# Kernel tuning notes

Measured on AMD Instinct MI355X. Metric: run time of the kernel, lower is better.

Reference implementation:

```python
import jax, jax.numpy as jnp
import numpy as np

T, B, IN, H, L = 512, 64, 1024, 1024, 2


def setup_inputs() -> dict:
    key = jax.random.key(0)
    ks = jax.random.split(key, 7)
    s = 1.0 / np.sqrt(H)
    return {
        "x": jax.random.normal(ks[0], (T, B, IN), jnp.float32),
        "h0": jax.random.normal(ks[1], (L, B, H), jnp.float32) * 0.1,
        "c0": jax.random.normal(ks[2], (L, B, H), jnp.float32) * 0.1,
        "W0": jax.random.uniform(ks[3], (4 * H, IN + H), jnp.float32, -s, s),
        "b0": jax.random.uniform(ks[4], (4 * H,), jnp.float32, -s, s),
        "W1": jax.random.uniform(ks[5], (4 * H, H + H), jnp.float32, -s, s),
        "b1": jax.random.uniform(ks[6], (4 * H,), jnp.float32, -s, s),
    }


def _cell(xin, h, c, W, b):
    # xin: [B, D], h/c: [B, H], W: [4H, D+H], b: [4H]
    xh = jnp.concatenate([xin, h], axis=1)
    gates = xh @ W.T + b
    i, f, g, o = jnp.split(gates, 4, axis=1)  # ingate, forgetgate, cellgate, outgate
    i = jax.nn.sigmoid(i)
    f = jax.nn.sigmoid(f)
    g = jnp.tanh(g)
    o = jax.nn.sigmoid(o)
    cy = i * g + f * c
    hy = o * jnp.tanh(cy)
    return hy, cy


def reference(x, h0, c0, W0, b0, W1, b1):
    Ws = [(W0, b0), (W1, b1)]

    def step(carry, xt):
        h, c = carry  # each [L, B, H]
        xin = xt
        hs, cs = [], []
        for k in range(L):
            W, b = Ws[k]
            hy, cy = _cell(xin, h[k], c[k], W, b)
            hs.append(hy)
            cs.append(cy)
            xin = hy
        return (jnp.stack(hs), jnp.stack(cs)), xin  # xin is last-layer h

    (h, c), hlast = jax.lax.scan(step, (h0, c0), x)
    return hlast, h, c
```

## Files before the change

### kernel.cpp

```cpp
#include <hip/hip_runtime.h>
#include <hip/hip_bf16.h>
#include <stdint.h>

#define TT 512
#define BB 64
#define HH 1024
#define BH 65536
#define KD 2048

typedef __attribute__((ext_vector_type(8))) short short8;
typedef __attribute__((ext_vector_type(4))) float f32x4;

__device__ __forceinline__ unsigned short f2bf(float f) {
  union { float f; unsigned int u; } v; v.f = f;
  unsigned int r = v.u + 0x7fffu + ((v.u >> 16) & 1u);
  return (unsigned short)(r >> 16);
}
__device__ __forceinline__ float bf2f(unsigned short u) {
  union { unsigned int u; float f; } v; v.u = ((unsigned int)u) << 16; return v.f;
}
__device__ __forceinline__ float fsig(float x)  { return 1.0f / (1.0f + __expf(-x)); }
__device__ __forceinline__ float ftanhf(float x){ return 1.0f - 2.0f / (__expf(2.0f * x) + 1.0f); }

__global__ void cvt_x_kernel(const float* __restrict__ x, unsigned short* __restrict__ xbf) {
  const int n4 = (TT * BB * 1024) / 4;
  int stride = gridDim.x * blockDim.x;
  for (int i = blockIdx.x * blockDim.x + threadIdx.x; i < n4; i += stride) {
    float4 v = ((const float4*)x)[i];
    unsigned long long p = (unsigned long long)f2bf(v.x)
        | ((unsigned long long)f2bf(v.y) << 16)
        | ((unsigned long long)f2bf(v.z) << 32)
        | ((unsigned long long)f2bf(v.w) << 48);
    ((unsigned long long*)xbf)[i] = p;
  }
}

__global__ void cvt_w_kernel(const float* __restrict__ W, unsigned short* __restrict__ Ws) {
  int idx = blockIdx.x * blockDim.x + threadIdx.x;
  int hi = idx & 3;
  int nr = (idx >> 2) & 31;
  int kk = (idx >> 7) & 63;
  int g  = idx >> 13;
  int q  = nr & 3;
  int jl = (nr >> 2) & 3;
  int nt = nr >> 4;
  int grow = (q << 10) + (g << 3) + (nt << 2) + jl;
  int k = ((kk < 32) ? (kk << 5) : (1024 + ((kk - 32) << 5))) + (hi << 3);
  const float* src = W + (size_t)grow * KD + k;
  float4 v0 = ((const float4*)src)[0];
  float4 v1 = ((const float4*)src)[1];
  unsigned long long p0 = (unsigned long long)f2bf(v0.x)
      | ((unsigned long long)f2bf(v0.y) << 16)
      | ((unsigned long long)f2bf(v0.z) << 32)
      | ((unsigned long long)f2bf(v0.w) << 48);
  unsigned long long p1 = (unsigned long long)f2bf(v1.x)
      | ((unsigned long long)f2bf(v1.y) << 16)
      | ((unsigned long long)f2bf(v1.z) << 32)
      | ((unsigned long long)f2bf(v1.w) << 48);
  unsigned long long* dst = (unsigned long long*)(Ws + ((size_t)g << 16) + (kk << 10) + (nr << 5) + (hi << 3));
  dst[0] = p0;
  dst[1] = p1;
}

__global__ void init_state_kernel(const float* __restrict__ h0in,
                                  unsigned short* h0s0, unsigned short* h1s0) {
  int i = blockIdx.x * blockDim.x + threadIdx.x;
  int m = i >> 10, c = i & 1023;
  int dst = ((c >> 3) << 9) + (m << 3) + (c & 7);
  h0s0[dst] = f2bf(h0in[i]);
  h1s0[dst] = f2bf(h0in[BH + i]);
}

__global__ void finalize_kernel(const unsigned short* __restrict__ h0hist,
                                const unsigned short* __restrict__ h1hist,
                                float* __restrict__ out) {
  const size_t NCH = (size_t)(TT + 2) * (BH / 8);
  size_t stride = (size_t)gridDim.x * blockDim.x;
  for (size_t i = (size_t)blockIdx.x * blockDim.x + threadIdx.x; i < NCH; i += stride) {
    int p  = (int)(i >> 13);
    int ci = (int)(i & 8191);
    int cb = ci >> 6, m = ci & 63;
    const unsigned short* src;
    size_t dbase;
    if (p < TT)       { src = h1hist + (size_t)(p + 1) * BH; dbase = (size_t)p * BH; }
    else if (p == TT) { src = h0hist + (size_t)TT * BH;      dbase = (size_t)TT * BH; }
    else              { src = h1hist + (size_t)TT * BH;      dbase = (size_t)TT * BH + BH; }
    const unsigned short* sp = src + ((size_t)ci << 3);
    ushort4 v0 = ((const ushort4*)sp)[0];
    ushort4 v1 = ((const ushort4*)sp)[1];
    float* dp = out + dbase + (m << 10) + (cb << 3);
    *(float4*)(dp)     = make_float4(bf2f(v0.x), bf2f(v0.y), bf2f(v0.z), bf2f(v0.w));
    *(float4*)(dp + 4) = make_float4(bf2f(v1.x), bf2f(v1.y), bf2f(v1.z), bf2f(v1.w));
  }
}

#define GLD(p)    __hip_atomic_load((p),  __ATOMIC_RELAXED, __HIP_MEMORY_SCOPE_AGENT)
#define GST(p, v) __hip_atomic_store((p), (v), __ATOMIC_RELAXED, __HIP_MEMORY_SCOPE_AGENT)

__device__ __forceinline__ void poll128(int* base) {
  for (;;) {
    int s = 0;
#pragma unroll
    for (int j = 0; j < 8; j++)
      s += GLD(base + (j << 6));
    if (s >= 128) return;
    __builtin_amdgcn_s_sleep(1);
  }
}

__global__ __launch_bounds__(512, 2) void lstm_persist(
    const unsigned short* __restrict__ W0s, const unsigned short* __restrict__ W1s,
    const float* __restrict__ b0, const float* __restrict__ b1,
    const unsigned short* __restrict__ xbf,
    unsigned short* h0hist, unsigned short* h1hist,
    const float* __restrict__ c0in, float* out, int* cnt)
{
  __shared__ short8 wlds[8192];
  __shared__ f32x4 pbuf[2][4][2][64];
  const int tid = threadIdx.x;
  const int bid = blockIdx.x;
  const int layer = bid >> 7;
  const int g = bid & 127;

  const unsigned short* Ws = layer ? W1s : W0s;
  const float* bias = layer ? b1 : b0;
  int* const cnt0 = cnt;
  int* const cnt1 = cnt + (TT << 9);

  {
    const short8* wsrc = (const short8*)(Ws + ((size_t)g << 16));
#pragma unroll
    for (int it = 0; it < 16; it++)
      wlds[tid + (it << 9)] = wsrc[tid + (it << 9)];
  }

  const int lane = tid & 63;
  const int w  = tid >> 6;
  const bool isA = (w < 4);
  const int mt = w & 3;
  const int m0 = mt << 4;
  const int n  = lane & 15;
  const int hi = lane >> 4;
  const short8* bbase0 = wlds + ((n << 2) + hi);
  const short8* bbase1 = wlds + (((16 + n) << 2) + hi);
  const int m = m0 + n;
  const int rowoff = (m << 10) + (hi << 3);
  const int bro = ((hi << 6) + m) << 3;
  const int col0 = (g << 3) + hi;
  const int col1 = col0 + 4;

  unsigned short* const myhist = (layer == 0) ? h0hist : h1hist;
  int* const mycnt = (layer == 0) ? cnt0 : cnt1;

  float bq[2][4];
  float creg[2];
  if (!isA) {
#pragma unroll
    for (int nt2 = 0; nt2 < 2; nt2++) {
      int col = nt2 ? col1 : col0;
#pragma unroll
      for (int qg = 0; qg < 4; qg++)
        bq[nt2][qg] = bias[(qg << 10) + col];
      creg[nt2] = c0in[(size_t)layer * BH + (m << 10) + col];
    }
  }
  __syncthreads();

  if (isA) {
    if (layer == 1) {
      if (lane == 0) poll128(cnt0);
      asm volatile("" ::: "memory");
    }
    f32x4 a0 = {0.f, 0.f, 0.f, 0.f}, a1 = {0.f, 0.f, 0.f, 0.f};
    if (layer == 0) {
      const unsigned short* asrc = xbf + rowoff;
      short8 ha[8];
#pragma unroll
      for (int j = 0; j < 8; j++) ha[j] = *(const short8*)(asrc + (j << 5));
#pragma unroll
      for (int blk = 0; blk < 4; blk++)
#pragma unroll
        for (int j = 0; j < 8; j++) {
          int kk = (blk << 3) + j;
          a0 = __builtin_amdgcn_mfma_f32_16x16x32_bf16(bbase0[kk << 7], ha[j], a0, 0, 0, 0);
          a1 = __builtin_amdgcn_mfma_f32_16x16x32_bf16(bbase1[kk << 7], ha[j], a1, 0, 0, 0);
          if (blk < 3) ha[j] = *(const short8*)(asrc + ((kk + 8) << 5));
        }
    } else {
      const unsigned short* asrc = h0hist + (size_t)BH + bro;
      short8 ha[8];
#pragma unroll
      for (int j = 0; j < 8; j++) ha[j] = *(const short8*)(asrc + (j << 11));
#pragma unroll
      for (int blk = 0; blk < 4; blk++)
#pragma unroll
        for (int j = 0; j < 8; j++) {
          int kk = (blk << 3) + j;
          a0 = __builtin_amdgcn_mfma_f32_16x16x32_bf16(bbase0[kk << 7], ha[j], a0, 0, 0, 0);
          a1 = __builtin_amdgcn_mfma_f32_16x16x32_bf16(bbase1[kk << 7], ha[j], a1, 0, 0, 0);
          if (blk < 3) ha[j] = *(const short8*)(asrc + ((kk + 8) << 11));
        }
    }
    pbuf[0][mt][0][lane] = a0;
    pbuf[0][mt][1][lane] = a1;
  }
  __syncthreads();

  for (int s = 0; s < TT; s++) {
    if (isA) {
      if (s + 1 < TT) {
        f32x4 a0 = {0.f, 0.f, 0.f, 0.f}, a1 = {0.f, 0.f, 0.f, 0.f};
        if (layer == 0) {
          const unsigned short* asrc = xbf + (size_t)(s + 1) * BH + rowoff;
          short8 ha[8];
#pragma unroll
          for (int j = 0; j < 8; j++) ha[j] = *(const short8*)(asrc + (j << 5));
#pragma unroll
          for (int blk = 0; blk < 4; blk++)
#pragma unroll
            for (int j = 0; j < 8; j++) {
              int kk = (blk << 3) + j;
              a0 = __builtin_amdgcn_mfma_f32_16x16x32_bf16(bbase0[kk << 7], ha[j], a0, 0, 0, 0);
              a1 = __builtin_amdgcn_mfma_f32_16x16x32_bf16(bbase1[kk << 7], ha[j], a1, 0, 0, 0);
              if (blk < 3) ha[j] = *(const short8*)(asrc + ((kk + 8) << 5));
            }
        } else {
          if (lane == 0) poll128(cnt0 + ((s + 1) << 9));
          asm volatile("" ::: "memory");
          const unsigned short* asrc = h0hist + (size_t)(s + 2) * BH + bro;
          short8 ha[8];
#pragma unroll
          for (int j = 0; j < 8; j++) ha[j] = *(const short8*)(asrc + (j << 11));
#pragma unroll
          for (int blk = 0; blk < 4; blk++)
#pragma unroll
            for (int j = 0; j < 8; j++) {
              int kk = (blk << 3) + j;
              a0 = __builtin_amdgcn_mfma_f32_16x16x32_bf16(bbase0[kk << 7], ha[j], a0, 0, 0, 0);
              a1 = __builtin_amdgcn_mfma_f32_16x16x32_bf16(bbase1[kk << 7], ha[j], a1, 0, 0, 0);
              if (blk < 3) ha[j] = *(const short8*)(asrc + ((kk + 8) << 11));
            }
        }
        int buf = (s + 1) & 1;
        pbuf[buf][mt][0][lane] = a0;
        pbuf[buf][mt][1][lane] = a1;
      }
    } else {
      if (s >= 1) {
        if (lane == 0) poll128(mycnt + ((s - 1) << 9));
        asm volatile("" ::: "memory");
      }
      f32x4 acc0 = pbuf[s & 1][mt][0][lane];
      f32x4 acc1 = pbuf[s & 1][mt][1][lane];
      const unsigned short* inB = myhist + (size_t)s * BH + bro;
      short8 ha[8];
#pragma unroll
      for (int j = 0; j < 8; j++) ha[j] = *(const short8*)(inB + (j << 11));
#pragma unroll
      for (int blk = 0; blk < 4; blk++)
#pragma unroll
        for (int j = 0; j < 8; j++) {
          int kk = (blk << 3) + j;
          acc0 = __builtin_amdgcn_mfma_f32_16x16x32_bf16(bbase0[(32 + kk) << 7], ha[j], acc0, 0, 0, 0);
          acc1 = __builtin_amdgcn_mfma_f32_16x16x32_bf16(bbase1[(32 + kk) << 7], ha[j], acc1, 0, 0, 0);
          if (blk < 3) ha[j] = *(const short8*)(inB + ((kk + 8) << 11));
        }

      unsigned short* hbb = myhist + (size_t)(s + 1) * BH + (((g << 6) + m) << 3);
#pragma unroll
      for (int nt2 = 0; nt2 < 2; nt2++) {
        f32x4 acc = nt2 ? acc1 : acc0;
        float ig = fsig(acc[0] + bq[nt2][0]);
        float fg = fsig(acc[1] + bq[nt2][1]);
        float gg = ftanhf(acc[2] + bq[nt2][2]);
        float og = fsig(acc[3] + bq[nt2][3]);
        float cn = ig * gg + fg * creg[nt2];
        float hn = og * ftanhf(cn);
        creg[nt2] = cn;
        GST(hbb + (nt2 << 2) + hi, f2bf(hn));
      }
    }

    __syncthreads();
    if (tid == 0) atomicAdd(mycnt + (s << 9) + ((g & 7) << 6), 1);

    if (!isA && s == TT - 1) {
#pragma unroll
      for (int nt2 = 0; nt2 < 2; nt2++) {
        const int col = nt2 ? col1 : col0;
        out[(size_t)TT * BH + (size_t)(2 + layer) * BH + (m << 10) + col] = creg[nt2];
      }
    }
  }
}

extern "C" void kernel_launch(void* const* d_in, const int* in_sizes, int n_in,
                              void* d_out, int out_size, void* d_ws, size_t ws_size,
                              hipStream_t stream) {
  (void)in_sizes; (void)n_in; (void)out_size; (void)ws_size;
  const float* x    = (const float*)d_in[0];
  const float* h0in = (const float*)d_in[1];
  const float* c0in = (const float*)d_in[2];
  const float* W0   = (const float*)d_in[3];
  const float* b0   = (const float*)d_in[4];
  const float* W1   = (const float*)d_in[5];
  const float* b1   = (const float*)d_in[6];
  float* out = (float*)d_out;

  char* ws = (char*)d_ws;
  const size_t HIST = (size_t)(TT + 1) * BH * sizeof(unsigned short);
  unsigned short* Xbf    = (unsigned short*)(ws);
  unsigned short* W0s    = (unsigned short*)(ws + 67108864);
  unsigned short* W1s    = (unsigned short*)(ws + 83886080);
  unsigned short* h0hist = (unsigned short*)(ws + 100663296);
  unsigned short* h1hist = (unsigned short*)(ws + 100663296 + HIST);
  int* cnt               = (int*)(ws + 100663296 + 2 * HIST);

  const size_t CNT_BYTES = (size_t)2 * TT * 512 * sizeof(int);
  hipMemsetAsync(cnt, 0, CNT_BYTES, stream);
  cvt_x_kernel<<<2048, 256, 0, stream>>>(x, Xbf);
  cvt_w_kernel<<<4096, 256, 0, stream>>>(W0, W0s);
  cvt_w_kernel<<<4096, 256, 0, stream>>>(W1, W1s);
  init_state_kernel<<<256, 256, 0, stream>>>(h0in, h0hist, h1hist);

  lstm_persist<<<256, 512, 0, stream>>>(W0s, W1s, b0, b1, Xbf,
                                        h0hist, h1hist, c0in, out, cnt);

  finalize_kernel<<<2048, 256, 0, stream>>>(h0hist, h1hist, out);
}
```

Before: 4.203 ms.

## Prefetch next-step A-wave inputs into registers and use a custom barrier

```diff
diff --git a/kernel.cpp b/kernel.cpp
--- a/kernel.cpp
+++ b/kernel.cpp
@@ -166,6 +166,7 @@
   }
   __syncthreads();
 
+  short8 xa[16], xb[16];
   if (isA) {
     if (layer == 1) {
       if (lane == 0) poll128(cnt0);
@@ -203,6 +204,21 @@
     }
     pbuf[0][mt][0][lane] = a0;
     pbuf[0][mt][1][lane] = a1;
+    if (layer == 0) {
+      const unsigned short* asrc = xbf + (size_t)BH + rowoff;
+#pragma unroll
+      for (int j = 0; j < 16; j++) xa[j] = *(const short8*)(asrc + (j << 5));
+#pragma unroll
+      for (int j = 0; j < 16; j++) xb[j] = *(const short8*)(asrc + ((16 + j) << 5));
+    } else {
+      if (lane == 0) poll128(cnt0 + (1 << 9));
+      asm volatile("" ::: "memory");
+      const unsigned short* asrc = h0hist + (size_t)2 * BH + bro;
+#pragma unroll
+      for (int j = 0; j < 16; j++) xa[j] = *(const short8*)(asrc + (j << 11));
+#pragma unroll
+      for (int j = 0; j < 16; j++) xb[j] = *(const short8*)(asrc + ((16 + j) << 11));
+    }
   }
   __syncthreads();
 
@@ -210,40 +226,36 @@
     if (isA) {
       if (s + 1 < TT) {
         f32x4 a0 = {0.f, 0.f, 0.f, 0.f}, a1 = {0.f, 0.f, 0.f, 0.f};
-        if (layer == 0) {
-          const unsigned short* asrc = xbf + (size_t)(s + 1) * BH + rowoff;
-          short8 ha[8];
-#pragma unroll
-          for (int j = 0; j < 8; j++) ha[j] = *(const short8*)(asrc + (j << 5));
-#pragma unroll
-          for (int blk = 0; blk < 4; blk++)
-#pragma unroll
-            for (int j = 0; j < 8; j++) {
-              int kk = (blk << 3) + j;
-              a0 = __builtin_amdgcn_mfma_f32_16x16x32_bf16(bbase0[kk << 7], ha[j], a0, 0, 0, 0);
-              a1 = __builtin_amdgcn_mfma_f32_16x16x32_bf16(bbase1[kk << 7], ha[j], a1, 0, 0, 0);
-              if (blk < 3) ha[j] = *(const short8*)(asrc + ((kk + 8) << 5));
-            }
-        } else {
-          if (lane == 0) poll128(cnt0 + ((s + 1) << 9));
-          asm volatile("" ::: "memory");
-          const unsigned short* asrc = h0hist + (size_t)(s + 2) * BH + bro;
-          short8 ha[8];
-#pragma unroll
-          for (int j = 0; j < 8; j++) ha[j] = *(const short8*)(asrc + (j << 11));
-#pragma unroll
-          for (int blk = 0; blk < 4; blk++)
-#pragma unroll
-            for (int j = 0; j < 8; j++) {
-              int kk = (blk << 3) + j;
-              a0 = __builtin_amdgcn_mfma_f32_16x16x32_bf16(bbase0[kk << 7], ha[j], a0, 0, 0, 0);
-              a1 = __builtin_amdgcn_mfma_f32_16x16x32_bf16(bbase1[kk << 7], ha[j], a1, 0, 0, 0);
-              if (blk < 3) ha[j] = *(const short8*)(asrc + ((kk + 8) << 11));
-            }
+#pragma unroll
+        for (int j = 0; j < 16; j++) {
+          a0 = __builtin_amdgcn_mfma_f32_16x16x32_bf16(bbase0[j << 7], xa[j], a0, 0, 0, 0);
+          a1 = __builtin_amdgcn_mfma_f32_16x16x32_bf16(bbase1[j << 7], xa[j], a1, 0, 0, 0);
+        }
+#pragma unroll
+        for (int j = 0; j < 16; j++) {
+          a0 = __builtin_amdgcn_mfma_f32_16x16x32_bf16(bbase0[(16 + j) << 7], xb[j], a0, 0, 0, 0);
+          a1 = __builtin_amdgcn_mfma_f32_16x16x32_bf16(bbase1[(16 + j) << 7], xb[j], a1, 0, 0, 0);
         }
         int buf = (s + 1) & 1;
         pbuf[buf][mt][0][lane] = a0;
         pbuf[buf][mt][1][lane] = a1;
+      }
+      if (s + 2 < TT) {
+        if (layer == 0) {
+          const unsigned short* asrc = xbf + (size_t)(s + 2) * BH + rowoff;
+#pragma unroll
+          for (int j = 0; j < 16; j++) xa[j] = *(const short8*)(asrc + (j << 5));
+#pragma unroll
+          for (int j = 0; j < 16; j++) xb[j] = *(const short8*)(asrc + ((16 + j) << 5));
+        } else {
+          if (lane == 0) poll128(cnt0 + ((s + 2) << 9));
+          asm volatile("" ::: "memory");
+          const unsigned short* asrc = h0hist + (size_t)(s + 3) * BH + bro;
+#pragma unroll
+          for (int j = 0; j < 16; j++) xa[j] = *(const short8*)(asrc + (j << 11));
+#pragma unroll
+          for (int j = 0; j < 16; j++) xb[j] = *(const short8*)(asrc + ((16 + j) << 11));
+        }
       }
     } else {
       if (s >= 1) {
@@ -279,10 +291,14 @@
         creg[nt2] = cn;
         GST(hbb + (nt2 << 2) + hi, f2bf(hn));
       }
-    }
-
-    __syncthreads();
-    if (tid == 0) atomicAdd(mycnt + (s << 9) + ((g & 7) << 6), 1);
+      asm volatile("s_waitcnt vmcnt(0)" ::: "memory");
+    }
+
+    asm volatile("s_waitcnt lgkmcnt(0)" ::: "memory");
+    __builtin_amdgcn_sched_barrier(0);
+    __builtin_amdgcn_s_barrier();
+    __builtin_amdgcn_sched_barrier(0);
+    if (tid == 256) atomicAdd(mycnt + (s << 9) + ((g & 7) << 6), 1);
 
     if (!isA && s == TT - 1) {
 #pragma unroll
```

After: 5.266 ms. 1.25x slower.

## Replace recurrent counter barrier with per-wave byte-tag flags and deepen load prefetch

Applied to the files above, without the earlier changes.

```diff
diff --git a/kernel.cpp b/kernel.cpp
--- a/kernel.cpp
+++ b/kernel.cpp
@@ -113,7 +113,7 @@
     const float* __restrict__ b0, const float* __restrict__ b1,
     const unsigned short* __restrict__ xbf,
     unsigned short* h0hist, unsigned short* h1hist,
-    const float* __restrict__ c0in, float* out, int* cnt)
+    const float* __restrict__ c0in, float* out, int* tags, int* cnt0)
 {
   __shared__ short8 wlds[8192];
   __shared__ f32x4 pbuf[2][4][2][64];
@@ -124,8 +124,7 @@
 
   const unsigned short* Ws = layer ? W1s : W0s;
   const float* bias = layer ? b1 : b0;
-  int* const cnt0 = cnt;
-  int* const cnt1 = cnt + (TT << 9);
+  int* const mytag = tags + (layer << 13);
 
   {
     const short8* wsrc = (const short8*)(Ws + ((size_t)g << 16));
@@ -150,7 +149,6 @@
   const int col1 = col0 + 4;
 
   unsigned short* const myhist = (layer == 0) ? h0hist : h1hist;
-  int* const mycnt = (layer == 0) ? cnt0 : cnt1;
 
   float bq[2][4];
   float creg[2];
@@ -212,59 +210,68 @@
         f32x4 a0 = {0.f, 0.f, 0.f, 0.f}, a1 = {0.f, 0.f, 0.f, 0.f};
         if (layer == 0) {
           const unsigned short* asrc = xbf + (size_t)(s + 1) * BH + rowoff;
-          short8 ha[8];
-#pragma unroll
-          for (int j = 0; j < 8; j++) ha[j] = *(const short8*)(asrc + (j << 5));
-#pragma unroll
-          for (int blk = 0; blk < 4; blk++)
-#pragma unroll
-            for (int j = 0; j < 8; j++) {
-              int kk = (blk << 3) + j;
-              a0 = __builtin_amdgcn_mfma_f32_16x16x32_bf16(bbase0[kk << 7], ha[j], a0, 0, 0, 0);
-              a1 = __builtin_amdgcn_mfma_f32_16x16x32_bf16(bbase1[kk << 7], ha[j], a1, 0, 0, 0);
-              if (blk < 3) ha[j] = *(const short8*)(asrc + ((kk + 8) << 5));
-            }
+          short8 ha[16];
+#pragma unroll
+          for (int j = 0; j < 16; j++) ha[j] = *(const short8*)(asrc + (j << 5));
+#pragma unroll
+          for (int j = 0; j < 16; j++) {
+            a0 = __builtin_amdgcn_mfma_f32_16x16x32_bf16(bbase0[j << 7], ha[j], a0, 0, 0, 0);
+            a1 = __builtin_amdgcn_mfma_f32_16x16x32_bf16(bbase1[j << 7], ha[j], a1, 0, 0, 0);
+            ha[j] = *(const short8*)(asrc + ((16 + j) << 5));
+          }
+#pragma unroll
+          for (int j = 0; j < 16; j++) {
+            a0 = __builtin_amdgcn_mfma_f32_16x16x32_bf16(bbase0[(16 + j) << 7], ha[j], a0, 0, 0, 0);
+            a1 = __builtin_amdgcn_mfma_f32_16x16x32_bf16(bbase1[(16 + j) << 7], ha[j], a1, 0, 0, 0);
+          }
         } else {
           if (lane == 0) poll128(cnt0 + ((s + 1) << 9));
           asm volatile("" ::: "memory");
           const unsigned short* asrc = h0hist + (size_t)(s + 2) * BH + bro;
-          short8 ha[8];
-#pragma unroll
-          for (int j = 0; j < 8; j++) ha[j] = *(const short8*)(asrc + (j << 11));
-#pragma unroll
-          for (int blk = 0; blk < 4; blk++)
-#pragma unroll
-            for (int j = 0; j < 8; j++) {
-              int kk = (blk << 3) + j;
-              a0 = __builtin_amdgcn_mfma_f32_16x16x32_bf16(bbase0[kk << 7], ha[j], a0, 0, 0, 0);
-              a1 = __builtin_amdgcn_mfma_f32_16x16x32_bf16(bbase1[kk << 7], ha[j], a1, 0, 0, 0);
-              if (blk < 3) ha[j] = *(const short8*)(asrc + ((kk + 8) << 11));
-            }
+          short8 ha[16];
+#pragma unroll
+          for (int j = 0; j < 16; j++) ha[j] = *(const short8*)(asrc + (j << 11));
+#pragma unroll
+          for (int j = 0; j < 16; j++) {
+            a0 = __builtin_amdgcn_mfma_f32_16x16x32_bf16(bbase0[j << 7], ha[j], a0, 0, 0, 0);
+            a1 = __builtin_amdgcn_mfma_f32_16x16x32_bf16(bbase1[j << 7], ha[j], a1, 0, 0, 0);
+            ha[j] = *(const short8*)(asrc + ((16 + j) << 11));
+          }
+#pragma unroll
+          for (int j = 0; j < 16; j++) {
+            a0 = __builtin_amdgcn_mfma_f32_16x16x32_bf16(bbase0[(16 + j) << 7], ha[j], a0, 0, 0, 0);
+            a1 = __builtin_amdgcn_mfma_f32_16x16x32_bf16(bbase1[(16 + j) << 7], ha[j], a1, 0, 0, 0);
+          }
         }
         int buf = (s + 1) & 1;
         pbuf[buf][mt][0][lane] = a0;
         pbuf[buf][mt][1][lane] = a1;
       }
     } else {
-      if (s >= 1) {
-        if (lane == 0) poll128(mycnt + ((s - 1) << 9));
+      {
+        const unsigned int expv = (unsigned int)(s & 255) * 0x01010101u;
+        const int* wp = mytag + ((((s & 3) << 2) + mt) << 9) + ((lane & 31) << 4);
+        unsigned int t = (unsigned int)GLD(wp);
+        while (t != expv) t = (unsigned int)GLD(wp);
         asm volatile("" ::: "memory");
       }
       f32x4 acc0 = pbuf[s & 1][mt][0][lane];
       f32x4 acc1 = pbuf[s & 1][mt][1][lane];
       const unsigned short* inB = myhist + (size_t)s * BH + bro;
-      short8 ha[8];
-#pragma unroll
-      for (int j = 0; j < 8; j++) ha[j] = *(const short8*)(inB + (j << 11));
-#pragma unroll
-      for (int blk = 0; blk < 4; blk++)
-#pragma unroll
-        for (int j = 0; j < 8; j++) {
-          int kk = (blk << 3) + j;
-          acc0 = __builtin_amdgcn_mfma_f32_16x16x32_bf16(bbase0[(32 + kk) << 7], ha[j], acc0, 0, 0, 0);
-          acc1 = __builtin_amdgcn_mfma_f32_16x16x32_bf16(bbase1[(32 + kk) << 7], ha[j], acc1, 0, 0, 0);
-          if (blk < 3) ha[j] = *(const short8*)(inB + ((kk + 8) << 11));
-        }
+      short8 ha[16];
+#pragma unroll
+      for (int j = 0; j < 16; j++) ha[j] = *(const short8*)(inB + (j << 11));
+#pragma unroll
+      for (int j = 0; j < 16; j++) {
+        acc0 = __builtin_amdgcn_mfma_f32_16x16x32_bf16(bbase0[(32 + j) << 7], ha[j], acc0, 0, 0, 0);
+        acc1 = __builtin_amdgcn_mfma_f32_16x16x32_bf16(bbase1[(32 + j) << 7], ha[j], acc1, 0, 0, 0);
+        ha[j] = *(const short8*)(inB + ((16 + j) << 11));
+      }
+#pragma unroll
+      for (int j = 0; j < 16; j++) {
+        acc0 = __builtin_amdgcn_mfma_f32_16x16x32_bf16(bbase0[(48 + j) << 7], ha[j], acc0, 0, 0, 0);
+        acc1 = __builtin_amdgcn_mfma_f32_16x16x32_bf16(bbase1[(48 + j) << 7], ha[j], acc1, 0, 0, 0);
+      }
 
       unsigned short* hbb = myhist + (size_t)(s + 1) * BH + (((g << 6) + m) << 3);
 #pragma unroll
@@ -279,10 +286,17 @@
         creg[nt2] = cn;
         GST(hbb + (nt2 << 2) + hi, f2bf(hn));
       }
+
+      asm volatile("s_waitcnt vmcnt(0)" ::: "memory");
+      if (lane == 0) {
+        unsigned char* tb = (unsigned char*)(mytag + (((((s + 1) & 3) << 2) + mt) << 9)
+                                             + ((g >> 2) << 4)) + (g & 3);
+        GST(tb, (unsigned char)((s + 1) & 255));
+      }
     }
 
     __syncthreads();
-    if (tid == 0) atomicAdd(mycnt + (s << 9) + ((g & 7) << 6), 1);
+    if (layer == 0 && tid == 0) atomicAdd(cnt0 + (s << 9) + ((g & 7) << 6), 1);
 
     if (!isA && s == TT - 1) {
 #pragma unroll
@@ -314,17 +328,18 @@
   unsigned short* W1s    = (unsigned short*)(ws + 83886080);
   unsigned short* h0hist = (unsigned short*)(ws + 100663296);
   unsigned short* h1hist = (unsigned short*)(ws + 100663296 + HIST);
-  int* cnt               = (int*)(ws + 100663296 + 2 * HIST);
-
-  const size_t CNT_BYTES = (size_t)2 * TT * 512 * sizeof(int);
-  hipMemsetAsync(cnt, 0, CNT_BYTES, stream);
+  int* tags              = (int*)(ws + 100663296 + 2 * HIST);
+  int* cnt0              = tags + 16384;
+
+  const size_t ZERO_BYTES = 65536 + (size_t)TT * 512 * sizeof(int);
+  hipMemsetAsync(tags, 0, ZERO_BYTES, stream);
   cvt_x_kernel<<<2048, 256, 0, stream>>>(x, Xbf);
   cvt_w_kernel<<<4096, 256, 0, stream>>>(W0, W0s);
   cvt_w_kernel<<<4096, 256, 0, stream>>>(W1, W1s);
   init_state_kernel<<<256, 256, 0, stream>>>(h0in, h0hist, h1hist);
 
   lstm_persist<<<256, 512, 0, stream>>>(W0s, W1s, b0, b1, Xbf,
-                                        h0hist, h1hist, c0in, out, cnt);
+                                        h0hist, h1hist, c0in, out, tags, cnt0);
 
   finalize_kernel<<<2048, 256, 0, stream>>>(h0hist, h1hist, out);
 }
```

Result: no change. 4.280 ms (+1.8%).

## Drop producer/consumer warp split; per-wave flags replace block barriers in LSTM loop

Applied to the files above, without the earlier changes.

```diff
diff --git a/kernel.cpp b/kernel.cpp
--- a/kernel.cpp
+++ b/kernel.cpp
@@ -113,10 +113,9 @@
     const float* __restrict__ b0, const float* __restrict__ b1,
     const unsigned short* __restrict__ xbf,
     unsigned short* h0hist, unsigned short* h1hist,
-    const float* __restrict__ c0in, float* out, int* cnt)
+    const float* __restrict__ c0in, float* out, int* cnt0m, int* cnt1m)
 {
   __shared__ short8 wlds[8192];
-  __shared__ f32x4 pbuf[2][4][2][64];
   const int tid = threadIdx.x;
   const int bid = blockIdx.x;
   const int layer = bid >> 7;
@@ -124,8 +123,6 @@
 
   const unsigned short* Ws = layer ? W1s : W0s;
   const float* bias = layer ? b1 : b0;
-  int* const cnt0 = cnt;
-  int* const cnt1 = cnt + (TT << 9);
 
   {
     const short8* wsrc = (const short8*)(Ws + ((size_t)g << 16));
@@ -133,11 +130,12 @@
     for (int it = 0; it < 16; it++)
       wlds[tid + (it << 9)] = wsrc[tid + (it << 9)];
   }
+  __syncthreads();
+  const int w = tid >> 6;
+  if (w >= 4) return;
 
   const int lane = tid & 63;
-  const int w  = tid >> 6;
-  const bool isA = (w < 4);
-  const int mt = w & 3;
+  const int mt = w;
   const int m0 = mt << 4;
   const int n  = lane & 15;
   const int hi = lane >> 4;
@@ -149,142 +147,86 @@
   const int col0 = (g << 3) + hi;
   const int col1 = col0 + 4;
 
-  unsigned short* const myhist = (layer == 0) ? h0hist : h1hist;
-  int* const mycnt = (layer == 0) ? cnt0 : cnt1;
+  unsigned short* const myhist = layer ? h1hist : h0hist;
+  int* const mycnt = layer ? cnt1m : cnt0m;
+  const unsigned short* const SAall = layer ? (h0hist + (size_t)BH) : xbf;
+  const int SAoff = layer ? bro : rowoff;
+  const int sash  = layer ? 11 : 5;
 
   float bq[2][4];
   float creg[2];
-  if (!isA) {
+#pragma unroll
+  for (int nt2 = 0; nt2 < 2; nt2++) {
+    int col = nt2 ? col1 : col0;
+#pragma unroll
+    for (int qg = 0; qg < 4; qg++)
+      bq[nt2][qg] = bias[(qg << 10) + col];
+    creg[nt2] = c0in[(size_t)layer * BH + (m << 10) + col];
+  }
+
+  for (int s = 0; s < TT; s++) {
+    if (layer) {
+      if (lane == 0) poll128(cnt0m + (((s << 2) + mt) << 9));
+      asm volatile("" ::: "memory");
+    }
+    const unsigned short* SA = SAall + (size_t)s * BH + SAoff;
+    short8 sa[16];
+#pragma unroll
+    for (int j = 0; j < 16; j++) sa[j] = *(const short8*)(SA + (j << sash));
+
+    if (s >= 1) {
+      if (lane == 0) poll128(mycnt + ((((s - 1) << 2) + mt) << 9));
+      asm volatile("" ::: "memory");
+    }
+    const unsigned short* SB = myhist + (size_t)s * BH + bro;
+    short8 sb[16], sc[16];
+#pragma unroll
+    for (int j = 0; j < 16; j++) sb[j] = *(const short8*)(SB + (j << 11));
+#pragma unroll
+    for (int j = 0; j < 16; j++) sc[j] = *(const short8*)(SB + ((16 + j) << 11));
+
+    f32x4 acc0 = {0.f, 0.f, 0.f, 0.f}, acc1 = {0.f, 0.f, 0.f, 0.f};
+#pragma unroll
+    for (int j = 0; j < 16; j++) {
+      acc0 = __builtin_amdgcn_mfma_f32_16x16x32_bf16(bbase0[j << 7], sa[j], acc0, 0, 0, 0);
+      acc1 = __builtin_amdgcn_mfma_f32_16x16x32_bf16(bbase1[j << 7], sa[j], acc1, 0, 0, 0);
+      sa[j] = *(const short8*)(SA + ((16 + j) << sash));
+    }
+#pragma unroll
+    for (int j = 0; j < 16; j++) {
+      acc0 = __builtin_amdgcn_mfma_f32_16x16x32_bf16(bbase0[(16 + j) << 7], sa[j], acc0, 0, 0, 0);
+      acc1 = __builtin_amdgcn_mfma_f32_16x16x32_bf16(bbase1[(16 + j) << 7], sa[j], acc1, 0, 0, 0);
+    }
+#pragma unroll
+    for (int j = 0; j < 16; j++) {
+      acc0 = __builtin_amdgcn_mfma_f32_16x16x32_bf16(bbase0[(32 + j) << 7], sb[j], acc0, 0, 0, 0);
+      acc1 = __builtin_amdgcn_mfma_f32_16x16x32_bf16(bbase1[(32 + j) << 7], sb[j], acc1, 0, 0, 0);
+    }
+#pragma unroll
+    for (int j = 0; j < 16; j++) {
+      acc0 = __builtin_amdgcn_mfma_f32_16x16x32_bf16(bbase0[(48 + j) << 7], sc[j], acc0, 0, 0, 0);
+      acc1 = __builtin_amdgcn_mfma_f32_16x16x32_bf16(bbase1[(48 + j) << 7], sc[j], acc1, 0, 0, 0);
+    }
+
+    unsigned short* hbb = myhist + (size_t)(s + 1) * BH + (((g << 6) + m) << 3);
 #pragma unroll
     for (int nt2 = 0; nt2 < 2; nt2++) {
-      int col = nt2 ? col1 : col0;
-#pragma unroll
-      for (int qg = 0; qg < 4; qg++)
-        bq[nt2][qg] = bias[(qg << 10) + col];
-      creg[nt2] = c0in[(size_t)layer * BH + (m << 10) + col];
-    }
-  }
-  __syncthreads();
-
-  if (isA) {
-    if (layer == 1) {
-      if (lane == 0) poll128(cnt0);
-      asm volatile("" ::: "memory");
-    }
-    f32x4 a0 = {0.f, 0.f, 0.f, 0.f}, a1 = {0.f, 0.f, 0.f, 0.f};
-    if (layer == 0) {
-      const unsigned short* asrc = xbf + rowoff;
-      short8 ha[8];
-#pragma unroll
-      for (int j = 0; j < 8; j++) ha[j] = *(const short8*)(asrc + (j << 5));
-#pragma unroll
-      for (int blk = 0; blk < 4; blk++)
-#pragma unroll
-        for (int j = 0; j < 8; j++) {
-          int kk = (blk << 3) + j;
-          a0 = __builtin_amdgcn_mfma_f32_16x16x32_bf16(bbase0[kk << 7], ha[j], a0, 0, 0, 0);
-          a1 = __builtin_amdgcn_mfma_f32_16x16x32_bf16(bbase1[kk << 7], ha[j], a1, 0, 0, 0);
-          if (blk < 3) ha[j] = *(const short8*)(asrc + ((kk + 8) << 5));
-        }
-    } else {
-      const unsigned short* asrc = h0hist + (size_t)BH + bro;
-      short8 ha[8];
-#pragma unroll
-      for (int j = 0; j < 8; j++) ha[j] = *(const short8*)(asrc + (j << 11));
-#pragma unroll
-      for (int blk = 0; blk < 4; blk++)
-#pragma unroll
-        for (int j = 0; j < 8; j++) {
-          int kk = (blk << 3) + j;
-          a0 = __builtin_amdgcn_mfma_f32_16x16x32_bf16(bbase0[kk << 7], ha[j], a0, 0, 0, 0);
-          a1 = __builtin_amdgcn_mfma_f32_16x16x32_bf16(bbase1[kk << 7], ha[j], a1, 0, 0, 0);
-          if (blk < 3) ha[j] = *(const short8*)(asrc + ((kk + 8) << 11));
-        }
-    }
-    pbuf[0][mt][0][lane] = a0;
-    pbuf[0][mt][1][lane] = a1;
-  }
-  __syncthreads();
-
-  for (int s = 0; s < TT; s++) {
-    if (isA) {
-      if (s + 1 < TT) {
-        f32x4 a0 = {0.f, 0.f, 0.f, 0.f}, a1 = {0.f, 0.f, 0.f, 0.f};
-        if (layer == 0) {
-          const unsigned short* asrc = xbf + (size_t)(s + 1) * BH + rowoff;
-          short8 ha[8];
-#pragma unroll
-          for (int j = 0; j < 8; j++) ha[j] = *(const short8*)(asrc + (j << 5));
-#pragma unroll
-          for (int blk = 0; blk < 4; blk++)
-#pragma unroll
-            for (int j = 0; j < 8; j++) {
-              int kk = (blk << 3) + j;
-              a0 = __builtin_amdgcn_mfma_f32_16x16x32_bf16(bbase0[kk << 7], ha[j], a0, 0, 0, 0);
-              a1 = __builtin_amdgcn_mfma_f32_16x16x32_bf16(bbase1[kk << 7], ha[j], a1, 0, 0, 0);
-              if (blk < 3) ha[j] = *(const short8*)(asrc + ((kk + 8) << 5));
-            }
-        } else {
-          if (lane == 0) poll128(cnt0 + ((s + 1) << 9));
-          asm volatile("" ::: "memory");
-          const unsigned short* asrc = h0hist + (size_t)(s + 2) * BH + bro;
-          short8 ha[8];
-#pragma unroll
-          for (int j = 0; j < 8; j++) ha[j] = *(const short8*)(asrc + (j << 11));
-#pragma unroll
-          for (int blk = 0; blk < 4; blk++)
-#pragma unroll
-            for (int j = 0; j < 8; j++) {
-              int kk = (blk << 3) + j;
-              a0 = __builtin_amdgcn_mfma_f32_16x16x32_bf16(bbase0[kk << 7], ha[j], a0, 0, 0, 0);
-              a1 = __builtin_amdgcn_mfma_f32_16x16x32_bf16(bbase1[kk << 7], ha[j], a1, 0, 0, 0);
-              if (blk < 3) ha[j] = *(const short8*)(asrc + ((kk + 8) << 11));
-            }
-        }
-        int buf = (s + 1) & 1;
-        pbuf[buf][mt][0][lane] = a0;
-        pbuf[buf][mt][1][lane] = a1;
-      }
-    } else {
-      if (s >= 1) {
-        if (lane == 0) poll128(mycnt + ((s - 1) << 9));
-        asm volatile("" ::: "memory");
-      }
-      f32x4 acc0 = pbuf[s & 1][mt][0][lane];
-      f32x4 acc1 = pbuf[s & 1][mt][1][lane];
-      const unsigned short* inB = myhist + (size_t)s * BH + bro;
-      short8 ha[8];
-#pragma unroll
-      for (int j = 0; j < 8; j++) ha[j] = *(const short8*)(inB + (j << 11));
-#pragma unroll
-      for (int blk = 0; blk < 4; blk++)
-#pragma unroll
-        for (int j = 0; j < 8; j++) {
-          int kk = (blk << 3) + j;
-          acc0 = __builtin_amdgcn_mfma_f32_16x16x32_bf16(bbase0[(32 + kk) << 7], ha[j], acc0, 0, 0, 0);
-          acc1 = __builtin_amdgcn_mfma_f32_16x16x32_bf16(bbase1[(32 + kk) << 7], ha[j], acc1, 0, 0, 0);
-          if (blk < 3) ha[j] = *(const short8*)(inB + ((kk + 8) << 11));
-        }
-
-      unsigned short* hbb = myhist + (size_t)(s + 1) * BH + (((g << 6) + m) << 3);
-#pragma unroll
-      for (int nt2 = 0; nt2 < 2; nt2++) {
-        f32x4 acc = nt2 ? acc1 : acc0;
-        float ig = fsig(acc[0] + bq[nt2][0]);
-        float fg = fsig(acc[1] + bq[nt2][1]);
-        float gg = ftanhf(acc[2] + bq[nt2][2]);
-        float og = fsig(acc[3] + bq[nt2][3]);
-        float cn = ig * gg + fg * creg[nt2];
-        float hn = og * ftanhf(cn);
-        creg[nt2] = cn;
-        GST(hbb + (nt2 << 2) + hi, f2bf(hn));
-      }
-    }
-
-    __syncthreads();
-    if (tid == 0) atomicAdd(mycnt + (s << 9) + ((g & 7) << 6), 1);
-
-    if (!isA && s == TT - 1) {
+      f32x4 acc = nt2 ? acc1 : acc0;
+      float ig = fsig(acc[0] + bq[nt2][0]);
+      float fg = fsig(acc[1] + bq[nt2][1]);
+      float gg = ftanhf(acc[2] + bq[nt2][2]);
+      float og = fsig(acc[3] + bq[nt2][3]);
+      float cn = ig * gg + fg * creg[nt2];
+      float hn = og * ftanhf(cn);
+      creg[nt2] = cn;
+      GST(hbb + (nt2 << 2) + hi, f2bf(hn));
+    }
+
+    asm volatile("s_waitcnt vmcnt(0)" ::: "memory");
+    if (lane == 0)
+      atomicAdd(mycnt + (((s << 2) + mt) << 9) + ((g & 7) << 6), 1);
+
+    if (s == TT - 1) {
 #pragma unroll
       for (int nt2 = 0; nt2 < 2; nt2++) {
         const int col = nt2 ? col1 : col0;
@@ -314,17 +256,17 @@
   unsigned short* W1s    = (unsigned short*)(ws + 83886080);
   unsigned short* h0hist = (unsigned short*)(ws + 100663296);
   unsigned short* h1hist = (unsigned short*)(ws + 100663296 + HIST);
-  int* cnt               = (int*)(ws + 100663296 + 2 * HIST);
-
-  const size_t CNT_BYTES = (size_t)2 * TT * 512 * sizeof(int);
-  hipMemsetAsync(cnt, 0, CNT_BYTES, stream);
+  int* cnt0m             = (int*)(ws + 100663296 + 2 * HIST);
+  int* cnt1m             = cnt0m + (1 << 20);
+
+  hipMemsetAsync(cnt0m, 0, (size_t)8 << 20, stream);
   cvt_x_kernel<<<2048, 256, 0, stream>>>(x, Xbf);
   cvt_w_kernel<<<4096, 256, 0, stream>>>(W0, W0s);
   cvt_w_kernel<<<4096, 256, 0, stream>>>(W1, W1s);
   init_state_kernel<<<256, 256, 0, stream>>>(h0in, h0hist, h1hist);
 
   lstm_persist<<<256, 512, 0, stream>>>(W0s, W1s, b0, b1, Xbf,
-                                        h0hist, h1hist, c0in, out, cnt);
+                                        h0hist, h1hist, c0in, out, cnt0m, cnt1m);
 
   finalize_kernel<<<2048, 256, 0, stream>>>(h0hist, h1hist, out);
 }
```

Result: slower. 7.465 ms (+77.6%).
